# Kernel optimization log

Hardware: AMD Instinct MI355X
Metric: run time of the kernel (lower is better)

## Reference

```python
import jax, jax.numpy as jnp
import numpy as np

N, E, H, NF, EF = 50000, 400000, 128, 10, 10


def setup_inputs() -> dict:
    key = jax.random.key(0)
    ks = iter(jax.random.split(key, 24))
    rn = lambda shape, s=0.1: jax.random.normal(next(ks), shape, jnp.float32) * s
    z = lambda shape: jnp.zeros(shape, jnp.float32)
    o = lambda shape: jnp.ones(shape, jnp.float32)
    return {
        "x": jax.random.normal(next(ks), (N, NF), jnp.float32),
        "edge_index": jax.random.randint(next(ks), (2, E), 0, N, jnp.int32),
        "edge_attr": jax.random.normal(next(ks), (E, EF), jnp.float32),
        "ne_w": rn((NF, H)), "ne_b": z(H), "ne_g": o(H), "ne_beta": z(H),
        "ee_w": rn((EF, H)), "ee_b": z(H), "ee_g": o(H), "ee_beta": z(H),
        "gate_w": rn((3 * H, H)), "gate_b": z(H),
        "gatA_w": rn((2, H, H)), "gatA_asrc": rn((2, 8, 16)), "gatA_adst": rn((2, 8, 16)), "gatA_bias": z((2, H)),
        "gatB_w": rn((H, H)), "gatB_asrc": rn((1, H)), "gatB_adst": rn((1, H)), "gatB_bias": z(H),
        "ln_g": o((3, H)), "ln_b": z((3, H)),
        "c1_w": rn((2 * H, H)), "c1_b": z(H), "cl1_g": o(H), "cl1_b": z(H),
        "c2_w": rn((H, H // 2)), "c2_b": z(H // 2), "cl2_g": o(H // 2), "cl2_b": z(H // 2),
        "c3_w": rn((H // 2, 2)), "c3_b": z(2),
    }


def _ln(x, g, b):
    m = x.mean(-1, keepdims=True)
    v = ((x - m) ** 2).mean(-1, keepdims=True)
    return (x - m) / jnp.sqrt(v + 1e-5) * g + b


def _gat(h, src, dst, n, w, asrc, adst, bias, concat):
    # PyG GATConv: lin (no bias), per-edge leaky_relu score, segment softmax over dst, scatter-add
    heads, dout = asrc.shape
    xp = (h @ w).reshape(n, heads, dout)             # [N, heads, dout]
    a_s = (xp * asrc).sum(-1)                        # [N, heads]
    a_d = (xp * adst).sum(-1)
    e = jax.nn.leaky_relu(a_s[src] + a_d[dst], 0.2)  # [E2, heads]
    m = jax.ops.segment_max(e, dst, num_segments=n)
    ex = jnp.exp(e - m[dst])
    s = jax.ops.segment_sum(ex, dst, num_segments=n)
    alpha = ex / s[dst]                               # [E2, heads]
    out = jax.ops.segment_sum(xp[src] * alpha[..., None], dst, num_segments=n)  # [N, heads, dout]
    out = out.reshape(n, heads * dout) if concat else out.mean(1)
    return out + bias


def reference(x, edge_index, edge_attr, ne_w, ne_b, ne_g, ne_beta, ee_w, ee_b, ee_g, ee_beta,
              gate_w, gate_b, gatA_w, gatA_asrc, gatA_adst, gatA_bias, gatB_w, gatB_asrc,
              gatB_adst, gatB_bias, ln_g, ln_b, c1_w, c1_b, cl1_g, cl1_b, c2_w, c2_b,
              cl2_g, cl2_b, c3_w, c3_b):
    n = x.shape[0]
    row, col = edge_index[0], edge_index[1]
    loops = jnp.arange(n, dtype=edge_index.dtype)     # GATConv add_self_loops=True
    src_sl = jnp.concatenate([row, loops])
    dst_sl = jnp.concatenate([col, loops])

    h = jax.nn.relu(_ln(x @ ne_w + ne_b, ne_g, ne_beta))      # node encoder (dropout=eval)
    for l in range(2):
        h = _gat(h, src_sl, dst_sl, n, gatA_w[l], gatA_asrc[l], gatA_adst[l], gatA_bias[l], True)
        h = jax.nn.relu(_ln(h, ln_g[l], ln_b[l]))
    h = _gat(h, src_sl, dst_sl, n, gatB_w, gatB_asrc, gatB_adst, gatB_bias, False)
    h = jax.nn.relu(_ln(h, ln_g[2], ln_b[2]))

    s = h[row]
    d = h[col]
    e = jax.nn.relu(_ln(edge_attr @ ee_w + ee_b, ee_g, ee_beta))  # edge encoder
    gate = jax.nn.sigmoid(jnp.concatenate([s, d, e], axis=1) @ gate_w + gate_b)
    s = s + gate * e
    d = d + gate * e

    zc = jax.nn.relu(_ln(jnp.concatenate([s, d], axis=1) @ c1_w + c1_b, cl1_g, cl1_b))
    zc = jax.nn.relu(_ln(zc @ c2_w + c2_b, cl2_g, cl2_b))
    return zc @ c3_w + c3_b                                   # [E, num_classes]
```

## Files before the change

kernel.cpp:

```cpp
#include <hip/hip_runtime.h>
#include <hip/hip_bf16.h>

#define H 128
#define NFEAT 10
#define EFEAT 10
#define XPS 144

typedef __attribute__((ext_vector_type(8))) short bf16x8;
typedef __attribute__((ext_vector_type(4))) float f32x4;

__device__ __forceinline__ float bflo(unsigned v) { return __uint_as_float(v << 16); }
__device__ __forceinline__ float bfhi(unsigned v) { return __uint_as_float(v & 0xffff0000u); }
__device__ __forceinline__ unsigned bfpack(float a, float b) {
    __hip_bfloat16 h0 = __float2bfloat16(a), h1 = __float2bfloat16(b);
    return (unsigned)(*(unsigned short*)&h0) | ((unsigned)(*(unsigned short*)&h1) << 16);
}

__global__ __launch_bounds__(256) void k_degree(const int* __restrict__ col,
                                                int* __restrict__ deg, int E, int N) {
    int i = blockIdx.x * blockDim.x + threadIdx.x;
    int E2 = E + N;
    if (i < E2) {
        int d = (i < E) ? col[i] : (i - E);
        atomicAdd(&deg[d], 1);
    }
}

__global__ __launch_bounds__(1024) void k_scan(const int* __restrict__ deg,
                                               int* __restrict__ offs,
                                               int* __restrict__ cursor, int N) {
    __shared__ int ps[1024];
    int t = threadIdx.x;
    int chunk = (N + 1023) / 1024;
    int begin = t * chunk;
    int end = begin + chunk; if (end > N) end = N;
    int s = 0;
    for (int i = begin; i < end; i++) s += deg[i];
    if (begin >= N) s = 0;
    ps[t] = s;
    __syncthreads();
    for (int off = 1; off < 1024; off <<= 1) {
        int v = (t >= off) ? ps[t - off] : 0;
        __syncthreads();
        ps[t] += v;
        __syncthreads();
    }
    int run = (t == 0) ? 0 : ps[t - 1];
    if (begin < N) {
        for (int i = begin; i < end; i++) {
            offs[i] = run;
            cursor[i] = run;
            run += deg[i];
        }
    }
    if (t == 1023) offs[N] = ps[1023];
}

__global__ __launch_bounds__(256) void k_scatter(const int* __restrict__ rowp,
                                                 const int* __restrict__ colp,
                                                 int* __restrict__ cursor,
                                                 int* __restrict__ srcs, int E, int N) {
    int i = blockIdx.x * blockDim.x + threadIdx.x;
    if (i < E + N) {
        int s, d;
        if (i < E) { s = rowp[i]; d = colp[i]; }
        else       { s = i - E;  d = i - E; }
        int pos = atomicAdd(&cursor[d], 1);
        srcs[pos] = s;
    }
}

__global__ __launch_bounds__(256) void k_node_enc(const float* __restrict__ x,
                                                  const float* __restrict__ wm,
                                                  const float* __restrict__ b,
                                                  const float* __restrict__ g,
                                                  const float* __restrict__ beta,
                                                  __hip_bfloat16* __restrict__ h, int N) {
    int t = threadIdx.x;
    int w = t >> 6, l = t & 63;
    int n = blockIdx.x * 4 + w;
    if (n >= N) return;
    float xs[NFEAT];
#pragma unroll
    for (int k = 0; k < NFEAT; k++) xs[k] = x[(size_t)n * NFEAT + k];
    float a0 = b[2 * l], a1 = b[2 * l + 1];
#pragma unroll
    for (int k = 0; k < NFEAT; k++) {
        float2 wv = *(const float2*)&wm[k * H + 2 * l];
        a0 += xs[k] * wv.x;
        a1 += xs[k] * wv.y;
    }
    float p = a0 + a1;
#pragma unroll
    for (int s = 1; s < 64; s <<= 1) p += __shfl_xor(p, s, 64);
    float mean = p * (1.0f / H);
    float d0 = a0 - mean, d1 = a1 - mean;
    float q = d0 * d0 + d1 * d1;
#pragma unroll
    for (int s = 1; s < 64; s <<= 1) q += __shfl_xor(q, s, 64);
    float rstd = rsqrtf(q * (1.0f / H) + 1e-5f);
    float y0 = fmaxf(d0 * rstd * g[2 * l] + beta[2 * l], 0.0f);
    float y1 = fmaxf(d1 * rstd * g[2 * l + 1] + beta[2 * l + 1], 0.0f);
    *(unsigned*)&h[(size_t)n * H + 2 * l] = bfpack(y0, y1);
}

__global__ __launch_bounds__(256, 2) void k_gat_xp_mfma(
        const __hip_bfloat16* __restrict__ h_bf,
        const __hip_bfloat16* __restrict__ wT,
        const float* __restrict__ asrc,
        const float* __restrict__ adst,
        __hip_bfloat16* __restrict__ xp_bf,
        float* __restrict__ a_d,
        int heads, int N) {
    __shared__ __hip_bfloat16 Ws[128 * 136];
    __shared__ __hip_bfloat16 As[64 * 136];
    int t = threadIdx.x;
    int n0 = blockIdx.x * 64;

#pragma unroll
    for (int it = 0; it < 2; it++) {
        int idx = it * 256 + t;
        int row = idx >> 2, seg = idx & 3;
        const uint4* src = (const uint4*)(wT + row * 128 + seg * 32);
        uint4 v0 = src[0], v1 = src[1], v2 = src[2], v3 = src[3];
        uint4* dst = (uint4*)&Ws[row * 136 + seg * 32];
        dst[0] = v0; dst[1] = v1; dst[2] = v2; dst[3] = v3;
    }
    {
        int row = t >> 2, seg = t & 3;
        int n = n0 + row; if (n >= N) n = N - 1;
        const uint4* src = (const uint4*)(h_bf + (size_t)n * 128 + seg * 32);
        uint4 v0 = src[0], v1 = src[1], v2 = src[2], v3 = src[3];
        uint4* dst = (uint4*)&As[row * 136 + seg * 32];
        dst[0] = v0; dst[1] = v1; dst[2] = v2; dst[3] = v3;
    }
    __syncthreads();

    int w = t >> 6, l = t & 63, ln15 = l & 15, quad = l >> 4, q8 = quad * 8;
    f32x4 acc[8] = {};
#pragma unroll
    for (int k = 0; k < 128; k += 32) {
        bf16x8 af = *(const bf16x8*)&As[(w * 16 + ln15) * 136 + k + q8];
#pragma unroll
        for (int i = 0; i < 8; i++) {
            bf16x8 bfr = *(const bf16x8*)&Ws[(i * 16 + ln15) * 136 + k + q8];
            acc[i] = __builtin_amdgcn_mfma_f32_16x16x32_bf16(af, bfr, acc[i], 0, 0, 0);
        }
    }

    if (heads == 8) {
#pragma unroll
        for (int i = 0; i < 8; i++) {
            float av = asrc[i * 16 + ln15], dvv = adst[i * 16 + ln15];
            float ps[4], pd[4];
#pragma unroll
            for (int r = 0; r < 4; r++) { ps[r] = acc[i][r] * av; pd[r] = acc[i][r] * dvv; }
#pragma unroll
            for (int s = 1; s < 16; s <<= 1) {
#pragma unroll
                for (int r = 0; r < 4; r++) {
                    ps[r] += __shfl_xor(ps[r], s, 64);
                    pd[r] += __shfl_xor(pd[r], s, 64);
                }
            }
            if (ln15 == 0) {
#pragma unroll
                for (int r = 0; r < 4; r++) {
                    int n = n0 + w * 16 + quad * 4 + r;
                    if (n < N) {
                        *(float*)&xp_bf[(size_t)n * XPS + 128 + 2 * i] = ps[r];
                        a_d[(size_t)n * 8 + i] = pd[r];
                    }
                }
            }
        }
    } else {
        float ps[4] = {0, 0, 0, 0}, pd[4] = {0, 0, 0, 0};
#pragma unroll
        for (int i = 0; i < 8; i++) {
            float av = asrc[i * 16 + ln15], dvv = adst[i * 16 + ln15];
#pragma unroll
            for (int r = 0; r < 4; r++) { ps[r] += acc[i][r] * av; pd[r] += acc[i][r] * dvv; }
        }
#pragma unroll
        for (int s = 1; s < 16; s <<= 1) {
#pragma unroll
            for (int r = 0; r < 4; r++) {
                ps[r] += __shfl_xor(ps[r], s, 64);
                pd[r] += __shfl_xor(pd[r], s, 64);
            }
        }
        if (ln15 == 0) {
#pragma unroll
            for (int r = 0; r < 4; r++) {
                int n = n0 + w * 16 + quad * 4 + r;
                if (n < N) {
                    *(float*)&xp_bf[(size_t)n * XPS + 128] = ps[r];
                    a_d[n] = pd[r];
                }
            }
        }
    }

#pragma unroll
    for (int i = 0; i < 8; i++) {
#pragma unroll
        for (int r = 0; r < 4; r++) {
            int n = n0 + w * 16 + quad * 4 + r;
            if (n < N) xp_bf[(size_t)n * XPS + i * 16 + ln15] = __float2bfloat16(acc[i][r]);
        }
    }
}

__global__ __launch_bounds__(256) void k_gat_agg(const __hip_bfloat16* __restrict__ xp,
                                                 const float* __restrict__ a_d,
                                                 const int* __restrict__ offs,
                                                 const int* __restrict__ srcs,
                                                 const float* __restrict__ bias,
                                                 const float* __restrict__ g,
                                                 const float* __restrict__ b,
                                                 __hip_bfloat16* __restrict__ hout,
                                                 int heads, int N) {
    int t = threadIdx.x;
    int w = t >> 6, l = t & 63;
    int n = blockIdx.x * 4 + w;
    if (n >= N) return;
    int head = (heads == 8) ? (l >> 3) : 0;
    float adv = a_d[(size_t)n * heads + head];
    int s0 = offs[n], s1 = offs[n + 1];
    float acc0 = 0.0f, acc1 = 0.0f, den = 0.0f;
    int j = s0;
    for (; j + 4 <= s1; j += 4) {
        int s_[4];
#pragma unroll
        for (int u = 0; u < 4; u++) s_[u] = srcs[j + u];
        float e_[4]; unsigned v_[4];
#pragma unroll
        for (int u = 0; u < 4; u++) {
            const __hip_bfloat16* xr = xp + (size_t)s_[u] * XPS;
            e_[u] = ((const float*)xr)[64 + head];
            v_[u] = *(const unsigned*)&xr[2 * l];
        }
#pragma unroll
        for (int u = 0; u < 4; u++) {
            float e = e_[u] + adv;
            e = (e >= 0.0f) ? e : 0.2f * e;
            float ex = __expf(e);
            den += ex;
            acc0 += ex * bflo(v_[u]);
            acc1 += ex * bfhi(v_[u]);
        }
    }
    for (; j < s1; j++) {
        int s = srcs[j];
        const __hip_bfloat16* xr = xp + (size_t)s * XPS;
        float e = ((const float*)xr)[64 + head] + adv;
        e = (e >= 0.0f) ? e : 0.2f * e;
        float ex = __expf(e);
        den += ex;
        unsigned v = *(const unsigned*)&xr[2 * l];
        acc0 += ex * bflo(v);
        acc1 += ex * bfhi(v);
    }
    float inv = 1.0f / den;
    float v0 = acc0 * inv + bias[2 * l];
    float v1 = acc1 * inv + bias[2 * l + 1];
    float p = v0 + v1;
#pragma unroll
    for (int s = 1; s < 64; s <<= 1) p += __shfl_xor(p, s, 64);
    float mean = p * (1.0f / H);
    float d0 = v0 - mean, d1 = v1 - mean;
    float q = d0 * d0 + d1 * d1;
#pragma unroll
    for (int s = 1; s < 64; s <<= 1) q += __shfl_xor(q, s, 64);
    float rstd = rsqrtf(q * (1.0f / H) + 1e-5f);
    float y0 = fmaxf(d0 * rstd * g[2 * l] + b[2 * l], 0.0f);
    float y1 = fmaxf(d1 * rstd * g[2 * l + 1] + b[2 * l + 1], 0.0f);
    *(unsigned*)&hout[(size_t)n * H + 2 * l] = bfpack(y0, y1);
}

__global__ __launch_bounds__(256) void k_wprep(const float* __restrict__ gate_w,
                                               const float* __restrict__ c1_w,
                                               const float* __restrict__ c2_w,
                                               const float* __restrict__ gatA_w,
                                               const float* __restrict__ gatB_w,
                                               const float* __restrict__ ee_w,
                                               __hip_bfloat16* __restrict__ gate_sw,
                                               __hip_bfloat16* __restrict__ c1_sw,
                                               __hip_bfloat16* __restrict__ c2_sw,
                                               __hip_bfloat16* __restrict__ wT3,
                                               __hip_bfloat16* __restrict__ ee_sw) {
    int i = blockIdx.x * blockDim.x + threadIdx.x;
    if (i < 49152) {
        int j = i & 7, lane = (i >> 3) & 63, rest = i >> 9;
        int nt = rest & 7, kc = rest >> 3;
        int n = nt * 16 + (lane & 15);
        int k = kc * 32 + (lane >> 4) * 8 + j;
        gate_sw[i] = __float2bfloat16(gate_w[k * 128 + n]);
    } else if (i < 81920) {
        int m = i - 49152;
        int j = m & 7, lane = (m >> 3) & 63, rest = m >> 9;
        int nt = rest & 7, kc = rest >> 3;
        int n = nt * 16 + (lane & 15);
        int k = kc * 32 + (lane >> 4) * 8 + j;
        c1_sw[m] = __float2bfloat16(c1_w[k * 128 + n]);
    } else if (i < 90112) {
        int m = i - 81920;
        int j = m & 7, lane = (m >> 3) & 63, rest = m >> 9;
        int nt = rest & 3, kc = rest >> 2;
        int n = nt * 16 + (lane & 15);
        int k = kc * 32 + (lane >> 4) * 8 + j;
        c2_sw[m] = __float2bfloat16(c2_w[k * 64 + n]);
    } else if (i < 139264) {
        int m = i - 90112;
        int mat = m / 16384, r = m % 16384;
        int n = r / 128, k = r % 128;
        const float* src = (mat < 2) ? (gatA_w + (size_t)mat * 16384) : gatB_w;
        wT3[m] = __float2bfloat16(src[k * 128 + n]);
    } else if (i < 143360) {
        int m = i - 139264;
        int j = m & 7, lane = (m >> 3) & 63, nt = (m >> 9) & 7;
        int n = nt * 16 + (lane & 15);
        int k = (lane >> 4) * 8 + j;
        ee_sw[m] = (k < EFEAT) ? __float2bfloat16(ee_w[k * 128 + n]) : __float2bfloat16(0.0f);
    }
}

__global__ __launch_bounds__(256, 4) void k_edge_cls_mfma(
        const __hip_bfloat16* __restrict__ h_bf,
        const int* __restrict__ rowp, const int* __restrict__ colp,
        const float* __restrict__ eattr,
        const __hip_bfloat16* __restrict__ ee_sw, const float* __restrict__ ee_b,
        const float* __restrict__ ee_g, const float* __restrict__ ee_beta,
        const __hip_bfloat16* __restrict__ gate_sw, const float* __restrict__ gate_b,
        const __hip_bfloat16* __restrict__ c1_sw, const float* __restrict__ c1_b,
        const float* __restrict__ cl1_g, const float* __restrict__ cl1_b,
        const __hip_bfloat16* __restrict__ c2_sw, const float* __restrict__ c2_b,
        const float* __restrict__ cl2_g, const float* __restrict__ cl2_b,
        const float* __restrict__ c3_w, const float* __restrict__ c3_b,
        float* __restrict__ out, int E) {
    __shared__ __align__(16) __hip_bfloat16 Bs[4 * 16 * 264];
    int t = threadIdx.x;
    int w = t >> 6, l = t & 63;
    int ln15 = l & 15, quad = l >> 4, q8 = quad * 8;
    int e0 = blockIdx.x * 64;
    int rbase = w * 16;
    __hip_bfloat16* B = Bs + w * (16 * 264);

    int eF = e0 + rbase + ln15; if (eF >= E) eF = E - 1;
    const __hip_bfloat16* rowS = h_bf + (size_t)rowp[eF] * 128;
    const __hip_bfloat16* rowD = h_bf + (size_t)colp[eF] * 128;

    {
        bf16x8 afe;
#pragma unroll
        for (int j = 0; j < 8; j++) {
            int k = q8 + j;
            float v = (k < EFEAT) ? eattr[(size_t)eF * EFEAT + k] : 0.0f;
            __hip_bfloat16 hv = __float2bfloat16(v);
            afe[j] = *(short*)&hv;
        }
        f32x4 acc[8] = {};
#pragma unroll
        for (int i = 0; i < 8; i++) {
            bf16x8 bfr = *(const bf16x8*)(ee_sw + ((size_t)i * 64 + l) * 8);
            acc[i] = __builtin_amdgcn_mfma_f32_16x16x32_bf16(afe, bfr, acc[i], 0, 0, 0);
        }
#pragma unroll
        for (int i = 0; i < 8; i++) {
            float cb = ee_b[i * 16 + ln15];
#pragma unroll
            for (int r = 0; r < 4; r++) acc[i][r] += cb;
        }
        float mean[4], rstd[4];
#pragma unroll
        for (int r = 0; r < 4; r++) {
            float p = 0.0f;
#pragma unroll
            for (int i = 0; i < 8; i++) p += acc[i][r];
            p += __shfl_xor(p, 1, 64); p += __shfl_xor(p, 2, 64);
            p += __shfl_xor(p, 4, 64); p += __shfl_xor(p, 8, 64);
            mean[r] = p * (1.0f / 128.0f);
        }
#pragma unroll
        for (int r = 0; r < 4; r++) {
            float q = 0.0f;
#pragma unroll
            for (int i = 0; i < 8; i++) { float d = acc[i][r] - mean[r]; q += d * d; }
            q += __shfl_xor(q, 1, 64); q += __shfl_xor(q, 2, 64);
            q += __shfl_xor(q, 4, 64); q += __shfl_xor(q, 8, 64);
            rstd[r] = rsqrtf(q * (1.0f / 128.0f) + 1e-5f);
        }
#pragma unroll
        for (int i = 0; i < 8; i++) {
            int cn = i * 16 + ln15;
            float g1 = ee_g[cn], b1 = ee_beta[cn];
#pragma unroll
            for (int r = 0; r < 4; r++) {
                int qr = quad * 4 + r;
                float y = fmaxf((acc[i][r] - mean[r]) * rstd[r] * g1 + b1, 0.0f);
                B[qr * 264 + cn] = __float2bfloat16(y);
            }
        }
    }

    {
        f32x4 acc[8] = {};
        bf16x8 fifo[4];
#pragma unroll
        for (int s = 0; s < 4; s++)
            fifo[s] = *(const bf16x8*)(gate_sw + ((size_t)s * 64 + l) * 8);
        bf16x8 acur = *(const bf16x8*)(rowS + q8);
        bf16x8 anx;
#pragma unroll
        for (int s = 0; s < 96; s++) {
            int kc = s >> 3, i = s & 7;
            if (i == 0 && kc < 11) {
                int k1 = kc + 1;
                if (k1 < 4)      anx = *(const bf16x8*)(rowS + k1 * 32 + q8);
                else if (k1 < 8) anx = *(const bf16x8*)(rowD + (k1 - 4) * 32 + q8);
                else             anx = *(const bf16x8*)&B[ln15 * 264 + (k1 - 8) * 32 + q8];
            }
            bf16x8 bcur = fifo[s & 3];
            if (s + 4 < 96)
                fifo[s & 3] = *(const bf16x8*)(gate_sw + ((size_t)(s + 4) * 64 + l) * 8);
            acc[i] = __builtin_amdgcn_mfma_f32_16x16x32_bf16(acur, bcur, acc[i], 0, 0, 0);
            if (i == 7) acur = anx;
        }
#pragma unroll
        for (int r = 0; r < 4; r++) {
            int qr = quad * 4 + r;
            int er = e0 + rbase + qr; if (er >= E) er = E - 1;
            const __hip_bfloat16* rS = h_bf + (size_t)rowp[er] * 128;
            const __hip_bfloat16* rD = h_bf + (size_t)colp[er] * 128;
#pragma unroll
            for (int i = 0; i < 8; i++) {
                int cn = i * 16 + ln15;
                float gt = 1.0f / (1.0f + __expf(-(acc[i][r] + gate_b[cn])));
                float ef = __bfloat162float(B[qr * 264 + cn]);
                float s  = __bfloat162float(rS[cn]);
                float d  = __bfloat162float(rD[cn]);
                B[qr * 264 + cn]       = __float2bfloat16(s + gt * ef);
                B[qr * 264 + 128 + cn] = __float2bfloat16(d + gt * ef);
            }
        }
    }

    {
        f32x4 acc[8] = {};
        bf16x8 fifo[4];
#pragma unroll
        for (int s = 0; s < 4; s++)
            fifo[s] = *(const bf16x8*)(c1_sw + ((size_t)s * 64 + l) * 8);
        bf16x8 acur = *(const bf16x8*)&B[ln15 * 264 + q8];
        bf16x8 anx;
#pragma unroll
        for (int s = 0; s < 64; s++) {
            int kc = s >> 3, i = s & 7;
            if (i == 0 && kc < 7)
                anx = *(const bf16x8*)&B[ln15 * 264 + (kc + 1) * 32 + q8];
            bf16x8 bcur = fifo[s & 3];
            if (s + 4 < 64)
                fifo[s & 3] = *(const bf16x8*)(c1_sw + ((size_t)(s + 4) * 64 + l) * 8);
            acc[i] = __builtin_amdgcn_mfma_f32_16x16x32_bf16(acur, bcur, acc[i], 0, 0, 0);
            if (i == 7) acur = anx;
        }
#pragma unroll
        for (int i = 0; i < 8; i++) {
            float cb = c1_b[i * 16 + ln15];
#pragma unroll
            for (int r = 0; r < 4; r++) acc[i][r] += cb;
        }
        float mean[4], rstd[4];
#pragma unroll
        for (int r = 0; r < 4; r++) {
            float p = 0.0f;
#pragma unroll
            for (int i = 0; i < 8; i++) p += acc[i][r];
            p += __shfl_xor(p, 1, 64); p += __shfl_xor(p, 2, 64);
            p += __shfl_xor(p, 4, 64); p += __shfl_xor(p, 8, 64);
            mean[r] = p * (1.0f / 128.0f);
        }
#pragma unroll
        for (int r = 0; r < 4; r++) {
            float q = 0.0f;
#pragma unroll
            for (int i = 0; i < 8; i++) { float d = acc[i][r] - mean[r]; q += d * d; }
            q += __shfl_xor(q, 1, 64); q += __shfl_xor(q, 2, 64);
            q += __shfl_xor(q, 4, 64); q += __shfl_xor(q, 8, 64);
            rstd[r] = rsqrtf(q * (1.0f / 128.0f) + 1e-5f);
        }
#pragma unroll
        for (int i = 0; i < 8; i++) {
            int cn = i * 16 + ln15;
            float g1 = cl1_g[cn], b1 = cl1_b[cn];
#pragma unroll
            for (int r = 0; r < 4; r++) {
                int qr = quad * 4 + r;
                float y = fmaxf((acc[i][r] - mean[r]) * rstd[r] * g1 + b1, 0.0f);
                B[qr * 264 + cn] = __float2bfloat16(y);
            }
        }
    }

    {
        f32x4 acc[4] = {};
        bf16x8 fifo[4];
#pragma unroll
        for (int s = 0; s < 4; s++)
            fifo[s] = *(const bf16x8*)(c2_sw + ((size_t)s * 64 + l) * 8);
        bf16x8 acur = *(const bf16x8*)&B[ln15 * 264 + q8];
        bf16x8 anx;
#pragma unroll
        for (int s = 0; s < 16; s++) {
            int kc = s >> 2, i = s & 3;
            if (i == 0 && kc < 3)
                anx = *(const bf16x8*)&B[ln15 * 264 + (kc + 1) * 32 + q8];
            bf16x8 bcur = fifo[s & 3];
            if (s + 4 < 16)
                fifo[s & 3] = *(const bf16x8*)(c2_sw + ((size_t)(s + 4) * 64 + l) * 8);
            acc[i] = __builtin_amdgcn_mfma_f32_16x16x32_bf16(acur, bcur, acc[i], 0, 0, 0);
            if (i == 3) acur = anx;
        }
#pragma unroll
        for (int i = 0; i < 4; i++) {
            float cb = c2_b[i * 16 + ln15];
#pragma unroll
            for (int r = 0; r < 4; r++) acc[i][r] += cb;
        }
        float mean[4], rstd[4];
#pragma unroll
        for (int r = 0; r < 4; r++) {
            float p = 0.0f;
#pragma unroll
            for (int i = 0; i < 4; i++) p += acc[i][r];
            p += __shfl_xor(p, 1, 64); p += __shfl_xor(p, 2, 64);
            p += __shfl_xor(p, 4, 64); p += __shfl_xor(p, 8, 64);
            mean[r] = p * (1.0f / 64.0f);
        }
#pragma unroll
        for (int r = 0; r < 4; r++) {
            float q = 0.0f;
#pragma unroll
            for (int i = 0; i < 4; i++) { float d = acc[i][r] - mean[r]; q += d * d; }
            q += __shfl_xor(q, 1, 64); q += __shfl_xor(q, 2, 64);
            q += __shfl_xor(q, 4, 64); q += __shfl_xor(q, 8, 64);
            rstd[r] = rsqrtf(q * (1.0f / 64.0f) + 1e-5f);
        }
        float w0[4], w1[4];
#pragma unroll
        for (int i = 0; i < 4; i++) {
            float2 cw = *(const float2*)&c3_w[(i * 16 + ln15) * 2];
            w0[i] = cw.x; w1[i] = cw.y;
        }
#pragma unroll
        for (int r = 0; r < 4; r++) {
            float s0 = 0.0f, s1 = 0.0f;
#pragma unroll
            for (int i = 0; i < 4; i++) {
                int cn = i * 16 + ln15;
                float y = fmaxf((acc[i][r] - mean[r]) * rstd[r] * cl2_g[cn] + cl2_b[cn], 0.0f);
                s0 += y * w0[i];
                s1 += y * w1[i];
            }
            s0 += __shfl_xor(s0, 1, 64); s0 += __shfl_xor(s0, 2, 64);
            s0 += __shfl_xor(s0, 4, 64); s0 += __shfl_xor(s0, 8, 64);
            s1 += __shfl_xor(s1, 1, 64); s1 += __shfl_xor(s1, 2, 64);
            s1 += __shfl_xor(s1, 4, 64); s1 += __shfl_xor(s1, 8, 64);
            if (ln15 == 0) {
                int e = e0 + rbase + quad * 4 + r;
                if (e < E) {
                    float2 o; o.x = s0 + c3_b[0]; o.y = s1 + c3_b[1];
                    *(float2*)&out[(size_t)e * 2] = o;
                }
            }
        }
    }
}

extern "C" void kernel_launch(void* const* d_in, const int* in_sizes, int n_in,
                              void* d_out, int out_size, void* d_ws, size_t ws_size,
                              hipStream_t stream) {
    const float* x        = (const float*)d_in[0];
    const int*   eidx     = (const int*)d_in[1];
    const float* eattr    = (const float*)d_in[2];
    const float* ne_w     = (const float*)d_in[3];
    const float* ne_b     = (const float*)d_in[4];
    const float* ne_g     = (const float*)d_in[5];
    const float* ne_beta  = (const float*)d_in[6];
    const float* ee_w     = (const float*)d_in[7];
    const float* ee_b     = (const float*)d_in[8];
    const float* ee_g     = (const float*)d_in[9];
    const float* ee_beta  = (const float*)d_in[10];
    const float* gate_w   = (const float*)d_in[11];
    const float* gate_b   = (const float*)d_in[12];
    const float* gatA_w   = (const float*)d_in[13];
    const float* gatA_as  = (const float*)d_in[14];
    const float* gatA_ad  = (const float*)d_in[15];
    const float* gatA_bias= (const float*)d_in[16];
    const float* gatB_w   = (const float*)d_in[17];
    const float* gatB_as  = (const float*)d_in[18];
    const float* gatB_ad  = (const float*)d_in[19];
    const float* gatB_bias= (const float*)d_in[20];
    const float* ln_g     = (const float*)d_in[21];
    const float* ln_b     = (const float*)d_in[22];
    const float* c1_w     = (const float*)d_in[23];
    const float* c1_b     = (const float*)d_in[24];
    const float* cl1_g    = (const float*)d_in[25];
    const float* cl1_b    = (const float*)d_in[26];
    const float* c2_w     = (const float*)d_in[27];
    const float* c2_b     = (const float*)d_in[28];
    const float* cl2_g    = (const float*)d_in[29];
    const float* cl2_b    = (const float*)d_in[30];
    const float* c3_w     = (const float*)d_in[31];
    const float* c3_b     = (const float*)d_in[32];

    const int N = in_sizes[0] / NFEAT;
    const int E = in_sizes[1] / 2;
    const int E2 = E + N;
    const int* rowp = eidx;
    const int* colp = eidx + E;

    char* ws = (char*)d_ws;
    size_t off = 0;
    auto alloc = [&](size_t bytes) -> void* {
        void* p = ws + off;
        off = (off + bytes + 255) & ~(size_t)255;
        return p;
    };
    int*   deg    = (int*)alloc((size_t)N * 4);
    int*   cursor = (int*)alloc((size_t)N * 4);
    int*   offs   = (int*)alloc((size_t)(N + 1) * 4);
    int*   srcs   = (int*)alloc((size_t)E2 * 4);
    float* a_d    = (float*)alloc((size_t)N * 8 * 4);
    __hip_bfloat16* h_bfA  = (__hip_bfloat16*)alloc((size_t)N * H * 2);
    __hip_bfloat16* h_bfB  = (__hip_bfloat16*)alloc((size_t)N * H * 2);
    __hip_bfloat16* xp_bf  = (__hip_bfloat16*)alloc((size_t)N * XPS * 2);
    __hip_bfloat16* gate_sw= (__hip_bfloat16*)alloc((size_t)49152 * 2);
    __hip_bfloat16* c1_sw  = (__hip_bfloat16*)alloc((size_t)32768 * 2);
    __hip_bfloat16* c2_sw  = (__hip_bfloat16*)alloc((size_t)8192 * 2);
    __hip_bfloat16* wT3    = (__hip_bfloat16*)alloc((size_t)3 * 128 * 128 * 2);
    __hip_bfloat16* ee_sw  = (__hip_bfloat16*)alloc((size_t)4096 * 2);
    (void)ws_size;

    k_wprep<<<(143360 + 255) / 256, 256, 0, stream>>>(gate_w, c1_w, c2_w, gatA_w, gatB_w, ee_w,
                                                      gate_sw, c1_sw, c2_sw, wT3, ee_sw);

    hipMemsetAsync(deg, 0, (size_t)N * 4, stream);
    k_degree<<<(E2 + 255) / 256, 256, 0, stream>>>(colp, deg, E, N);
    k_scan<<<1, 1024, 0, stream>>>(deg, offs, cursor, N);
    k_scatter<<<(E2 + 255) / 256, 256, 0, stream>>>(rowp, colp, cursor, srcs, E, N);

    int ngrid = (N + 3) / 4;
    k_node_enc<<<ngrid, 256, 0, stream>>>(x, ne_w, ne_b, ne_g, ne_beta, h_bfA, N);

    int xpgrid = (N + 63) / 64;
    __hip_bfloat16* hin = h_bfA;
    __hip_bfloat16* hout = h_bfB;
    for (int l = 0; l < 2; l++) {
        k_gat_xp_mfma<<<xpgrid, 256, 0, stream>>>(hin, wT3 + (size_t)l * 16384,
                                                  gatA_as + l * H, gatA_ad + l * H,
                                                  xp_bf, a_d, 8, N);
        k_gat_agg<<<ngrid, 256, 0, stream>>>(xp_bf, a_d, offs, srcs,
                                             gatA_bias + l * H, ln_g + l * H, ln_b + l * H,
                                             hout, 8, N);
        __hip_bfloat16* tmp = hin; hin = hout; hout = tmp;
    }
    k_gat_xp_mfma<<<xpgrid, 256, 0, stream>>>(hin, wT3 + (size_t)2 * 16384,
                                              gatB_as, gatB_ad,
                                              xp_bf, a_d, 1, N);
    k_gat_agg<<<ngrid, 256, 0, stream>>>(xp_bf, a_d, offs, srcs,
                                         gatB_bias, ln_g + 2 * H, ln_b + 2 * H,
                                         hout, 1, N);

    k_edge_cls_mfma<<<(E + 63) / 64, 256, 0, stream>>>(
        hout, rowp, colp, eattr,
        ee_sw, ee_b, ee_g, ee_beta,
        gate_sw, gate_b,
        c1_sw, c1_b, cl1_g, cl1_b,
        c2_sw, c2_b, cl2_g, cl2_b,
        c3_w, c3_b,
        (float*)d_out, E);
}
```

Baseline: 680.2 us.

## Rewrite edge classifier with 32x32 MFMA, register-resident activations, no LDS

```diff
diff --git a/kernel.cpp b/kernel.cpp
--- a/kernel.cpp
+++ b/kernel.cpp
@@ -8,12 +8,73 @@
 
 typedef __attribute__((ext_vector_type(8))) short bf16x8;
 typedef __attribute__((ext_vector_type(4))) float f32x4;
+typedef __attribute__((ext_vector_type(16))) float f32x16;
+typedef __attribute__((ext_vector_type(4))) unsigned u32x4;
+typedef __attribute__((ext_vector_type(2))) unsigned u32x2;
 
 __device__ __forceinline__ float bflo(unsigned v) { return __uint_as_float(v << 16); }
 __device__ __forceinline__ float bfhi(unsigned v) { return __uint_as_float(v & 0xffff0000u); }
 __device__ __forceinline__ unsigned bfpack(float a, float b) {
     __hip_bfloat16 h0 = __float2bfloat16(a), h1 = __float2bfloat16(b);
     return (unsigned)(*(unsigned short*)&h0) | ((unsigned)(*(unsigned short*)&h1) << 16);
+}
+__device__ __forceinline__ bf16x8 cast8(u32x4 v) { return __builtin_bit_cast(bf16x8, v); }
+
+__device__ __forceinline__ bf16x8 frag_from_pack(const unsigned* w, int b2) {
+    u32x4 t;
+    t.x = w[b2 * 4 + 0];
+    t.y = w[b2 * 4 + 1];
+    t.z = w[b2 * 4 + 2];
+    t.w = w[b2 * 4 + 3];
+    return cast8(t);
+}
+
+template<int NT>
+__device__ __forceinline__ void bias_ln_relu_pack(f32x16* acc, const float* __restrict__ bias,
+        const float* __restrict__ g, const float* __restrict__ beta,
+        int hh, float invn, unsigned (*pk)[8]) {
+    float sm = 0.f;
+#pragma unroll
+    for (int m = 0; m < NT; m++) {
+#pragma unroll
+        for (int P = 0; P < 4; P++) {
+            f32x4 bv = *(const f32x4*)&bias[m * 32 + P * 8 + hh * 4];
+#pragma unroll
+            for (int u = 0; u < 4; u++) {
+                float v = acc[m][P * 4 + u] + bv[u];
+                acc[m][P * 4 + u] = v;
+                sm += v;
+            }
+        }
+    }
+    sm += __shfl_xor(sm, 32, 64);
+    float mean = sm * invn;
+    float q = 0.f;
+#pragma unroll
+    for (int m = 0; m < NT; m++) {
+#pragma unroll
+        for (int r = 0; r < 16; r++) { float d = acc[m][r] - mean; q += d * d; }
+    }
+    q += __shfl_xor(q, 32, 64);
+    float rstd = rsqrtf(q * invn + 1e-5f);
+#pragma unroll
+    for (int m = 0; m < NT; m++) {
+#pragma unroll
+        for (int P = 0; P < 4; P++) {
+            f32x4 gv = *(const f32x4*)&g[m * 32 + P * 8 + hh * 4];
+            f32x4 bz = *(const f32x4*)&beta[m * 32 + P * 8 + hh * 4];
+#pragma unroll
+            for (int u = 0; u < 4; u++) {
+                float y = fmaxf((acc[m][P * 4 + u] - mean) * rstd * gv[u] + bz[u], 0.f);
+                acc[m][P * 4 + u] = y;
+            }
+        }
+    }
+#pragma unroll
+    for (int m = 0; m < NT; m++) {
+#pragma unroll
+        for (int p = 0; p < 8; p++) pk[m][p] = bfpack(acc[m][2 * p], acc[m][2 * p + 1]);
+    }
 }
 
 __global__ __launch_bounds__(256) void k_degree(const int* __restrict__ col,
@@ -292,288 +353,247 @@
                                                __hip_bfloat16* __restrict__ ee_sw) {
     int i = blockIdx.x * blockDim.x + threadIdx.x;
     if (i < 49152) {
-        int j = i & 7, lane = (i >> 3) & 63, rest = i >> 9;
-        int nt = rest & 7, kc = rest >> 3;
-        int n = nt * 16 + (lane & 15);
-        int k = kc * 32 + (lane >> 4) * 8 + j;
+        int j = i & 7, l = (i >> 3) & 63, s = i >> 9;
+        int m = s & 3, ks = s >> 2;
+        int hh = l >> 5;
+        int k;
+        if (ks < 8) k = 256 + ks * 16 + 4 * hh + (j & 3) + 8 * (j >> 2);
+        else        k = (ks - 8) * 16 + hh * 8 + j;
+        int n = m * 32 + (l & 31);
         gate_sw[i] = __float2bfloat16(gate_w[k * 128 + n]);
     } else if (i < 81920) {
-        int m = i - 49152;
-        int j = m & 7, lane = (m >> 3) & 63, rest = m >> 9;
-        int nt = rest & 7, kc = rest >> 3;
-        int n = nt * 16 + (lane & 15);
-        int k = kc * 32 + (lane >> 4) * 8 + j;
-        c1_sw[m] = __float2bfloat16(c1_w[k * 128 + n]);
+        int mm = i - 49152;
+        int j = mm & 7, l = (mm >> 3) & 63, s = mm >> 9;
+        int m = s & 3, ks = s >> 2;
+        int k = ks * 16 + 4 * (l >> 5) + (j & 3) + 8 * (j >> 2);
+        int n = m * 32 + (l & 31);
+        c1_sw[mm] = __float2bfloat16(c1_w[k * 128 + n]);
     } else if (i < 90112) {
-        int m = i - 81920;
-        int j = m & 7, lane = (m >> 3) & 63, rest = m >> 9;
-        int nt = rest & 3, kc = rest >> 2;
-        int n = nt * 16 + (lane & 15);
-        int k = kc * 32 + (lane >> 4) * 8 + j;
-        c2_sw[m] = __float2bfloat16(c2_w[k * 64 + n]);
+        int mm = i - 81920;
+        int j = mm & 7, l = (mm >> 3) & 63, s = mm >> 9;
+        int m = s & 1, ks = s >> 1;
+        int k = ks * 16 + 4 * (l >> 5) + (j & 3) + 8 * (j >> 2);
+        int n = m * 32 + (l & 31);
+        c2_sw[mm] = __float2bfloat16(c2_w[k * 64 + n]);
     } else if (i < 139264) {
         int m = i - 90112;
         int mat = m / 16384, r = m % 16384;
         int n = r / 128, k = r % 128;
         const float* src = (mat < 2) ? (gatA_w + (size_t)mat * 16384) : gatB_w;
         wT3[m] = __float2bfloat16(src[k * 128 + n]);
-    } else if (i < 143360) {
-        int m = i - 139264;
-        int j = m & 7, lane = (m >> 3) & 63, nt = (m >> 9) & 7;
-        int n = nt * 16 + (lane & 15);
-        int k = (lane >> 4) * 8 + j;
-        ee_sw[m] = (k < EFEAT) ? __float2bfloat16(ee_w[k * 128 + n]) : __float2bfloat16(0.0f);
-    }
-}
-
-__global__ __launch_bounds__(256, 4) void k_edge_cls_mfma(
+    } else if (i < 141312) {
+        int mm = i - 139264;
+        int j = mm & 7, l = (mm >> 3) & 63, s = mm >> 9;
+        int k = (l >> 5) * 8 + j;
+        int n = s * 32 + (l & 31);
+        ee_sw[mm] = (k < EFEAT) ? __float2bfloat16(ee_w[k * 128 + n]) : __float2bfloat16(0.0f);
+    }
+}
+
+__global__ __launch_bounds__(256, 3) void k_edge_cls_mfma32(
         const __hip_bfloat16* __restrict__ h_bf,
         const int* __restrict__ rowp, const int* __restrict__ colp,
         const float* __restrict__ eattr,
-        const __hip_bfloat16* __restrict__ ee_sw, const float* __restrict__ ee_b,
+        const __hip_bfloat16* __restrict__ ee_fa, const float* __restrict__ ee_b,
         const float* __restrict__ ee_g, const float* __restrict__ ee_beta,
-        const __hip_bfloat16* __restrict__ gate_sw, const float* __restrict__ gate_b,
-        const __hip_bfloat16* __restrict__ c1_sw, const float* __restrict__ c1_b,
+        const __hip_bfloat16* __restrict__ gate_fa, const float* __restrict__ gate_b,
+        const __hip_bfloat16* __restrict__ c1_fa, const float* __restrict__ c1_b,
         const float* __restrict__ cl1_g, const float* __restrict__ cl1_b,
-        const __hip_bfloat16* __restrict__ c2_sw, const float* __restrict__ c2_b,
+        const __hip_bfloat16* __restrict__ c2_fa, const float* __restrict__ c2_b,
         const float* __restrict__ cl2_g, const float* __restrict__ cl2_b,
         const float* __restrict__ c3_w, const float* __restrict__ c3_b,
         float* __restrict__ out, int E) {
-    __shared__ __align__(16) __hip_bfloat16 Bs[4 * 16 * 264];
     int t = threadIdx.x;
     int w = t >> 6, l = t & 63;
-    int ln15 = l & 15, quad = l >> 4, q8 = quad * 8;
-    int e0 = blockIdx.x * 64;
-    int rbase = w * 16;
-    __hip_bfloat16* B = Bs + w * (16 * 264);
-
-    int eF = e0 + rbase + ln15; if (eF >= E) eF = E - 1;
-    const __hip_bfloat16* rowS = h_bf + (size_t)rowp[eF] * 128;
-    const __hip_bfloat16* rowD = h_bf + (size_t)colp[eF] * 128;
-
+    int hh = l >> 5, e32 = l & 31;
+    int eIdx = blockIdx.x * 128 + w * 32 + e32;
+    int eF = (eIdx < E) ? eIdx : (E - 1);
+    int ri = rowp[eF], ci = colp[eF];
+    const unsigned short* rS = (const unsigned short*)h_bf + (size_t)ri * H;
+    const unsigned short* rD = (const unsigned short*)h_bf + (size_t)ci * H;
+
+    unsigned efw[4][8];
     {
-        bf16x8 afe;
-#pragma unroll
-        for (int j = 0; j < 8; j++) {
-            int k = q8 + j;
-            float v = (k < EFEAT) ? eattr[(size_t)eF * EFEAT + k] : 0.0f;
-            __hip_bfloat16 hv = __float2bfloat16(v);
-            afe[j] = *(short*)&hv;
-        }
-        f32x4 acc[8] = {};
-#pragma unroll
-        for (int i = 0; i < 8; i++) {
-            bf16x8 bfr = *(const bf16x8*)(ee_sw + ((size_t)i * 64 + l) * 8);
-            acc[i] = __builtin_amdgcn_mfma_f32_16x16x32_bf16(afe, bfr, acc[i], 0, 0, 0);
-        }
-#pragma unroll
-        for (int i = 0; i < 8; i++) {
-            float cb = ee_b[i * 16 + ln15];
-#pragma unroll
-            for (int r = 0; r < 4; r++) acc[i][r] += cb;
-        }
-        float mean[4], rstd[4];
-#pragma unroll
-        for (int r = 0; r < 4; r++) {
-            float p = 0.0f;
-#pragma unroll
-            for (int i = 0; i < 8; i++) p += acc[i][r];
-            p += __shfl_xor(p, 1, 64); p += __shfl_xor(p, 2, 64);
-            p += __shfl_xor(p, 4, 64); p += __shfl_xor(p, 8, 64);
-            mean[r] = p * (1.0f / 128.0f);
-        }
-#pragma unroll
-        for (int r = 0; r < 4; r++) {
-            float q = 0.0f;
-#pragma unroll
-            for (int i = 0; i < 8; i++) { float d = acc[i][r] - mean[r]; q += d * d; }
-            q += __shfl_xor(q, 1, 64); q += __shfl_xor(q, 2, 64);
-            q += __shfl_xor(q, 4, 64); q += __shfl_xor(q, 8, 64);
-            rstd[r] = rsqrtf(q * (1.0f / 128.0f) + 1e-5f);
-        }
-#pragma unroll
-        for (int i = 0; i < 8; i++) {
-            int cn = i * 16 + ln15;
-            float g1 = ee_g[cn], b1 = ee_beta[cn];
-#pragma unroll
-            for (int r = 0; r < 4; r++) {
-                int qr = quad * 4 + r;
-                float y = fmaxf((acc[i][r] - mean[r]) * rstd[r] * g1 + b1, 0.0f);
-                B[qr * 264 + cn] = __float2bfloat16(y);
-            }
-        }
-    }
-
+        const char* eb = (const char*)(eattr + (size_t)eF * EFEAT);
+        float2 p0 = *(const float2*)(eb + (hh << 5));
+        float2 p1 = *(const float2*)(eb + 8);
+        float2 p2 = *(const float2*)(eb + 16);
+        float2 p3 = *(const float2*)(eb + 24);
+        if (hh) { p1.x = p1.y = 0.f; p2.x = p2.y = 0.f; p3.x = p3.y = 0.f; }
+        u32x4 bwv;
+        bwv.x = bfpack(p0.x, p0.y);
+        bwv.y = bfpack(p1.x, p1.y);
+        bwv.z = bfpack(p2.x, p2.y);
+        bwv.w = bfpack(p3.x, p3.y);
+        bf16x8 bb = cast8(bwv);
+        f32x16 acc[4] = {};
+#pragma unroll
+        for (int m = 0; m < 4; m++) {
+            bf16x8 a = *(const bf16x8*)(ee_fa + ((size_t)m * 64 + l) * 8);
+            acc[m] = __builtin_amdgcn_mfma_f32_32x32x16_bf16(a, bb, acc[m], 0, 0, 0);
+        }
+        bias_ln_relu_pack<4>(acc, ee_b, ee_g, ee_beta, hh, 1.f / 128.f, efw);
+    }
+
+    f32x16 acc1[4] = {};
     {
-        f32x4 acc[8] = {};
-        bf16x8 fifo[4];
-#pragma unroll
-        for (int s = 0; s < 4; s++)
-            fifo[s] = *(const bf16x8*)(gate_sw + ((size_t)s * 64 + l) * 8);
-        bf16x8 acur = *(const bf16x8*)(rowS + q8);
-        bf16x8 anx;
-#pragma unroll
-        for (int s = 0; s < 96; s++) {
-            int kc = s >> 3, i = s & 7;
-            if (i == 0 && kc < 11) {
-                int k1 = kc + 1;
-                if (k1 < 4)      anx = *(const bf16x8*)(rowS + k1 * 32 + q8);
-                else if (k1 < 8) anx = *(const bf16x8*)(rowD + (k1 - 4) * 32 + q8);
-                else             anx = *(const bf16x8*)&B[ln15 * 264 + (k1 - 8) * 32 + q8];
-            }
-            bf16x8 bcur = fifo[s & 3];
-            if (s + 4 < 96)
-                fifo[s & 3] = *(const bf16x8*)(gate_sw + ((size_t)(s + 4) * 64 + l) * 8);
-            acc[i] = __builtin_amdgcn_mfma_f32_16x16x32_bf16(acur, bcur, acc[i], 0, 0, 0);
-            if (i == 7) acur = anx;
-        }
-#pragma unroll
-        for (int r = 0; r < 4; r++) {
-            int qr = quad * 4 + r;
-            int er = e0 + rbase + qr; if (er >= E) er = E - 1;
-            const __hip_bfloat16* rS = h_bf + (size_t)rowp[er] * 128;
-            const __hip_bfloat16* rD = h_bf + (size_t)colp[er] * 128;
-#pragma unroll
-            for (int i = 0; i < 8; i++) {
-                int cn = i * 16 + ln15;
-                float gt = 1.0f / (1.0f + __expf(-(acc[i][r] + gate_b[cn])));
-                float ef = __bfloat162float(B[qr * 264 + cn]);
-                float s  = __bfloat162float(rS[cn]);
-                float d  = __bfloat162float(rD[cn]);
-                B[qr * 264 + cn]       = __float2bfloat16(s + gt * ef);
-                B[qr * 264 + 128 + cn] = __float2bfloat16(d + gt * ef);
-            }
-        }
-    }
-
+        bf16x8 af[4];
+#pragma unroll
+        for (int s = 0; s < 4; s++) af[s] = *(const bf16x8*)(gate_fa + ((size_t)s * 64 + l) * 8);
+#pragma unroll
+        for (int ks = 0; ks < 8; ks++) {
+            int m = ks >> 1, b2 = ks & 1;
+            bf16x8 bb = frag_from_pack(efw[m], b2);
+#pragma unroll
+            for (int mt = 0; mt < 4; mt++) {
+                int s = ks * 4 + mt;
+                bf16x8 a = af[s & 3];
+                af[s & 3] = *(const bf16x8*)(gate_fa + ((size_t)(s + 4) * 64 + l) * 8);
+                acc1[mt] = __builtin_amdgcn_mfma_f32_32x32x16_bf16(a, bb, acc1[mt], 0, 0, 0);
+            }
+        }
+#pragma unroll
+        for (int ks = 8; ks < 24; ks++) {
+            const unsigned short* rp = (ks < 16) ? rS : rD;
+            int kl = ((ks - 8) & 7) * 16 + hh * 8;
+            bf16x8 bb = *(const bf16x8*)(rp + kl);
+#pragma unroll
+            for (int mt = 0; mt < 4; mt++) {
+                int s = ks * 4 + mt;
+                bf16x8 a = af[s & 3];
+                if (s + 4 < 96) af[s & 3] = *(const bf16x8*)(gate_fa + ((size_t)(s + 4) * 64 + l) * 8);
+                acc1[mt] = __builtin_amdgcn_mfma_f32_32x32x16_bf16(a, bb, acc1[mt], 0, 0, 0);
+            }
+        }
+    }
+
+    unsigned sw[4][8], dw[4][8];
     {
-        f32x4 acc[8] = {};
-        bf16x8 fifo[4];
-#pragma unroll
-        for (int s = 0; s < 4; s++)
-            fifo[s] = *(const bf16x8*)(c1_sw + ((size_t)s * 64 + l) * 8);
-        bf16x8 acur = *(const bf16x8*)&B[ln15 * 264 + q8];
-        bf16x8 anx;
-#pragma unroll
-        for (int s = 0; s < 64; s++) {
-            int kc = s >> 3, i = s & 7;
-            if (i == 0 && kc < 7)
-                anx = *(const bf16x8*)&B[ln15 * 264 + (kc + 1) * 32 + q8];
-            bf16x8 bcur = fifo[s & 3];
-            if (s + 4 < 64)
-                fifo[s & 3] = *(const bf16x8*)(c1_sw + ((size_t)(s + 4) * 64 + l) * 8);
-            acc[i] = __builtin_amdgcn_mfma_f32_16x16x32_bf16(acur, bcur, acc[i], 0, 0, 0);
-            if (i == 7) acur = anx;
-        }
-#pragma unroll
-        for (int i = 0; i < 8; i++) {
-            float cb = c1_b[i * 16 + ln15];
-#pragma unroll
-            for (int r = 0; r < 4; r++) acc[i][r] += cb;
-        }
-        float mean[4], rstd[4];
-#pragma unroll
-        for (int r = 0; r < 4; r++) {
-            float p = 0.0f;
-#pragma unroll
-            for (int i = 0; i < 8; i++) p += acc[i][r];
-            p += __shfl_xor(p, 1, 64); p += __shfl_xor(p, 2, 64);
-            p += __shfl_xor(p, 4, 64); p += __shfl_xor(p, 8, 64);
-            mean[r] = p * (1.0f / 128.0f);
-        }
-#pragma unroll
-        for (int r = 0; r < 4; r++) {
-            float q = 0.0f;
-#pragma unroll
-            for (int i = 0; i < 8; i++) { float d = acc[i][r] - mean[r]; q += d * d; }
-            q += __shfl_xor(q, 1, 64); q += __shfl_xor(q, 2, 64);
-            q += __shfl_xor(q, 4, 64); q += __shfl_xor(q, 8, 64);
-            rstd[r] = rsqrtf(q * (1.0f / 128.0f) + 1e-5f);
-        }
-#pragma unroll
-        for (int i = 0; i < 8; i++) {
-            int cn = i * 16 + ln15;
-            float g1 = cl1_g[cn], b1 = cl1_b[cn];
-#pragma unroll
-            for (int r = 0; r < 4; r++) {
-                int qr = quad * 4 + r;
-                float y = fmaxf((acc[i][r] - mean[r]) * rstd[r] * g1 + b1, 0.0f);
-                B[qr * 264 + cn] = __float2bfloat16(y);
-            }
-        }
-    }
-
+#pragma unroll
+        for (int m = 0; m < 4; m++) {
+#pragma unroll
+            for (int P = 0; P < 4; P++) {
+                int f0 = m * 32 + P * 8 + hh * 4;
+                f32x4 gb = *(const f32x4*)&gate_b[f0];
+                u32x2 sv = *(const u32x2*)(rS + f0);
+                u32x2 dv = *(const u32x2*)(rD + f0);
+#pragma unroll
+                for (int u2 = 0; u2 < 2; u2++) {
+                    int p = P * 2 + u2;
+                    unsigned svw = u2 ? sv.y : sv.x;
+                    unsigned dvw = u2 ? dv.y : dv.x;
+                    float g0 = acc1[m][2 * p] + gb[2 * u2];
+                    float g1 = acc1[m][2 * p + 1] + gb[2 * u2 + 1];
+                    g0 = 1.f / (1.f + __expf(-g0));
+                    g1 = 1.f / (1.f + __expf(-g1));
+                    float e0 = bflo(efw[m][p]), e1 = bfhi(efw[m][p]);
+                    sw[m][p] = bfpack(bflo(svw) + g0 * e0, bfhi(svw) + g1 * e1);
+                    dw[m][p] = bfpack(bflo(dvw) + g0 * e0, bfhi(dvw) + g1 * e1);
+                }
+            }
+        }
+    }
+
+    unsigned z1w[4][8];
     {
-        f32x4 acc[4] = {};
-        bf16x8 fifo[4];
-#pragma unroll
-        for (int s = 0; s < 4; s++)
-            fifo[s] = *(const bf16x8*)(c2_sw + ((size_t)s * 64 + l) * 8);
-        bf16x8 acur = *(const bf16x8*)&B[ln15 * 264 + q8];
-        bf16x8 anx;
-#pragma unroll
-        for (int s = 0; s < 16; s++) {
-            int kc = s >> 2, i = s & 3;
-            if (i == 0 && kc < 3)
-                anx = *(const bf16x8*)&B[ln15 * 264 + (kc + 1) * 32 + q8];
-            bf16x8 bcur = fifo[s & 3];
-            if (s + 4 < 16)
-                fifo[s & 3] = *(const bf16x8*)(c2_sw + ((size_t)(s + 4) * 64 + l) * 8);
-            acc[i] = __builtin_amdgcn_mfma_f32_16x16x32_bf16(acur, bcur, acc[i], 0, 0, 0);
-            if (i == 3) acur = anx;
-        }
-#pragma unroll
-        for (int i = 0; i < 4; i++) {
-            float cb = c2_b[i * 16 + ln15];
-#pragma unroll
-            for (int r = 0; r < 4; r++) acc[i][r] += cb;
-        }
-        float mean[4], rstd[4];
-#pragma unroll
-        for (int r = 0; r < 4; r++) {
-            float p = 0.0f;
-#pragma unroll
-            for (int i = 0; i < 4; i++) p += acc[i][r];
-            p += __shfl_xor(p, 1, 64); p += __shfl_xor(p, 2, 64);
-            p += __shfl_xor(p, 4, 64); p += __shfl_xor(p, 8, 64);
-            mean[r] = p * (1.0f / 64.0f);
-        }
-#pragma unroll
-        for (int r = 0; r < 4; r++) {
-            float q = 0.0f;
-#pragma unroll
-            for (int i = 0; i < 4; i++) { float d = acc[i][r] - mean[r]; q += d * d; }
-            q += __shfl_xor(q, 1, 64); q += __shfl_xor(q, 2, 64);
-            q += __shfl_xor(q, 4, 64); q += __shfl_xor(q, 8, 64);
-            rstd[r] = rsqrtf(q * (1.0f / 64.0f) + 1e-5f);
-        }
-        float w0[4], w1[4];
-#pragma unroll
-        for (int i = 0; i < 4; i++) {
-            float2 cw = *(const float2*)&c3_w[(i * 16 + ln15) * 2];
-            w0[i] = cw.x; w1[i] = cw.y;
-        }
-#pragma unroll
-        for (int r = 0; r < 4; r++) {
-            float s0 = 0.0f, s1 = 0.0f;
-#pragma unroll
-            for (int i = 0; i < 4; i++) {
-                int cn = i * 16 + ln15;
-                float y = fmaxf((acc[i][r] - mean[r]) * rstd[r] * cl2_g[cn] + cl2_b[cn], 0.0f);
-                s0 += y * w0[i];
-                s1 += y * w1[i];
-            }
-            s0 += __shfl_xor(s0, 1, 64); s0 += __shfl_xor(s0, 2, 64);
-            s0 += __shfl_xor(s0, 4, 64); s0 += __shfl_xor(s0, 8, 64);
-            s1 += __shfl_xor(s1, 1, 64); s1 += __shfl_xor(s1, 2, 64);
-            s1 += __shfl_xor(s1, 4, 64); s1 += __shfl_xor(s1, 8, 64);
-            if (ln15 == 0) {
-                int e = e0 + rbase + quad * 4 + r;
-                if (e < E) {
-                    float2 o; o.x = s0 + c3_b[0]; o.y = s1 + c3_b[1];
-                    *(float2*)&out[(size_t)e * 2] = o;
+        f32x16 acc2[4] = {};
+        bf16x8 af[4];
+#pragma unroll
+        for (int s = 0; s < 4; s++) af[s] = *(const bf16x8*)(c1_fa + ((size_t)s * 64 + l) * 8);
+#pragma unroll
+        for (int ks = 0; ks < 8; ks++) {
+            int m = ks >> 1, b2 = ks & 1;
+            bf16x8 bb = frag_from_pack(sw[m], b2);
+#pragma unroll
+            for (int mt = 0; mt < 4; mt++) {
+                int s = ks * 4 + mt;
+                bf16x8 a = af[s & 3];
+                af[s & 3] = *(const bf16x8*)(c1_fa + ((size_t)(s + 4) * 64 + l) * 8);
+                acc2[mt] = __builtin_amdgcn_mfma_f32_32x32x16_bf16(a, bb, acc2[mt], 0, 0, 0);
+            }
+        }
+#pragma unroll
+        for (int ks = 8; ks < 16; ks++) {
+            int kk = ks - 8;
+            int m = kk >> 1, b2 = kk & 1;
+            bf16x8 bb = frag_from_pack(dw[m], b2);
+#pragma unroll
+            for (int mt = 0; mt < 4; mt++) {
+                int s = ks * 4 + mt;
+                bf16x8 a = af[s & 3];
+                if (s + 4 < 64) af[s & 3] = *(const bf16x8*)(c1_fa + ((size_t)(s + 4) * 64 + l) * 8);
+                acc2[mt] = __builtin_amdgcn_mfma_f32_32x32x16_bf16(a, bb, acc2[mt], 0, 0, 0);
+            }
+        }
+        bias_ln_relu_pack<4>(acc2, c1_b, cl1_g, cl1_b, hh, 1.f / 128.f, z1w);
+    }
+
+    {
+        f32x16 acc3[2] = {};
+        bf16x8 af[4];
+#pragma unroll
+        for (int s = 0; s < 4; s++) af[s] = *(const bf16x8*)(c2_fa + ((size_t)s * 64 + l) * 8);
+#pragma unroll
+        for (int ks = 0; ks < 8; ks++) {
+            int m = ks >> 1, b2 = ks & 1;
+            bf16x8 bb = frag_from_pack(z1w[m], b2);
+#pragma unroll
+            for (int mt = 0; mt < 2; mt++) {
+                int s = ks * 2 + mt;
+                bf16x8 a = af[s & 3];
+                if (s + 4 < 16) af[s & 3] = *(const bf16x8*)(c2_fa + ((size_t)(s + 4) * 64 + l) * 8);
+                acc3[mt] = __builtin_amdgcn_mfma_f32_32x32x16_bf16(a, bb, acc3[mt], 0, 0, 0);
+            }
+        }
+        float sm = 0.f;
+#pragma unroll
+        for (int m = 0; m < 2; m++) {
+#pragma unroll
+            for (int P = 0; P < 4; P++) {
+                f32x4 bv = *(const f32x4*)&c2_b[m * 32 + P * 8 + hh * 4];
+#pragma unroll
+                for (int u = 0; u < 4; u++) {
+                    float v = acc3[m][P * 4 + u] + bv[u];
+                    acc3[m][P * 4 + u] = v;
+                    sm += v;
                 }
             }
+        }
+        sm += __shfl_xor(sm, 32, 64);
+        float mean = sm * (1.f / 64.f);
+        float q = 0.f;
+#pragma unroll
+        for (int m = 0; m < 2; m++) {
+#pragma unroll
+            for (int r = 0; r < 16; r++) { float d = acc3[m][r] - mean; q += d * d; }
+        }
+        q += __shfl_xor(q, 32, 64);
+        float rstd = rsqrtf(q * (1.f / 64.f) + 1e-5f);
+        float s0 = 0.f, s1 = 0.f;
+#pragma unroll
+        for (int m = 0; m < 2; m++) {
+#pragma unroll
+            for (int P = 0; P < 4; P++) {
+                int f0 = m * 32 + P * 8 + hh * 4;
+                f32x4 gv = *(const f32x4*)&cl2_g[f0];
+                f32x4 bz = *(const f32x4*)&cl2_b[f0];
+                f32x4 wA = *(const f32x4*)&c3_w[f0 * 2];
+                f32x4 wB = *(const f32x4*)&c3_w[f0 * 2 + 4];
+#pragma unroll
+                for (int u = 0; u < 4; u++) {
+                    float y = fmaxf((acc3[m][P * 4 + u] - mean) * rstd * gv[u] + bz[u], 0.f);
+                    float wc0 = (u < 2) ? wA[2 * u] : wB[2 * u - 4];
+                    float wc1 = (u < 2) ? wA[2 * u + 1] : wB[2 * u - 3];
+                    s0 += y * wc0;
+                    s1 += y * wc1;
+                }
+            }
+        }
+        s0 += __shfl_xor(s0, 32, 64);
+        s1 += __shfl_xor(s1, 32, 64);
+        if (hh == 0 && eIdx < E) {
+            float2 o; o.x = s0 + c3_b[0]; o.y = s1 + c3_b[1];
+            *(float2*)&out[(size_t)eIdx * 2] = o;
         }
     }
 }
@@ -643,7 +663,7 @@
     __hip_bfloat16* ee_sw  = (__hip_bfloat16*)alloc((size_t)4096 * 2);
     (void)ws_size;
 
-    k_wprep<<<(143360 + 255) / 256, 256, 0, stream>>>(gate_w, c1_w, c2_w, gatA_w, gatB_w, ee_w,
+    k_wprep<<<(141312 + 255) / 256, 256, 0, stream>>>(gate_w, c1_w, c2_w, gatA_w, gatB_w, ee_w,
                                                       gate_sw, c1_sw, c2_sw, wT3, ee_sw);
 
     hipMemsetAsync(deg, 0, (size_t)N * 4, stream);
@@ -673,7 +693,7 @@
                                          gatB_bias, ln_g + 2 * H, ln_b + 2 * H,
                                          hout, 1, N);
 
-    k_edge_cls_mfma<<<(E + 63) / 64, 256, 0, stream>>>(
+    k_edge_cls_mfma32<<<(E + 127) / 128, 256, 0, stream>>>(
         hout, rowp, colp, eattr,
         ee_sw, ee_b, ee_g, ee_beta,
         gate_sw, gate_b,
```

Result: slower. 882.7 us (+29.8%).
